# Performance work log

Measured on AMD Instinct MI355X. Metric: run time of the kernel, lower is better.

## Reference

```python
import jax, jax.numpy as jnp
import numpy as np

B, C, H, W = 2, 512, 128, 128
L_NUM, HEADS, LEVELS, POINTS = 6, 8, 1, 4
HEAD_DIM = C // HEADS


def setup_inputs() -> dict:
    key = jax.random.key(0)
    ks = jax.random.split(key, 16)
    s = 0.02
    rn = lambda k, shape, scale=s: jax.random.normal(k, shape, jnp.float32) * scale
    return dict(
        bev_feat=jax.random.normal(ks[0], (B, C, H, W), jnp.float32),
        lidar_feat=jax.random.normal(ks[1], (B, C, H, W), jnp.float32),
        Wv=rn(ks[2], (L_NUM, C, C)), bv=jnp.zeros((L_NUM, C), jnp.float32),
        Woff=rn(ks[3], (L_NUM, C, HEADS * LEVELS * POINTS * 2)),
        boff=rn(ks[4], (L_NUM, HEADS * LEVELS * POINTS * 2), 0.5),
        Waw=rn(ks[5], (L_NUM, C, HEADS * LEVELS * POINTS)),
        baw=jnp.zeros((L_NUM, HEADS * LEVELS * POINTS), jnp.float32),
        Wout=rn(ks[6], (L_NUM, C, C)), bout=jnp.zeros((L_NUM, C), jnp.float32),
        ln1_g=jnp.ones((L_NUM, C), jnp.float32), ln1_b=jnp.zeros((L_NUM, C), jnp.float32),
        W1=rn(ks[7], (L_NUM, C, C)), W2=rn(ks[8], (L_NUM, C, C)),
        ln2_g=jnp.ones((L_NUM, C), jnp.float32), ln2_b=jnp.zeros((L_NUM, C), jnp.float32),
        pe_W1=rn(ks[9], (2, C), 0.5),
        pe_bn_g=jnp.ones((C,), jnp.float32), pe_bn_b=jnp.zeros((C,), jnp.float32),
        pe_bn_m=jnp.zeros((C,), jnp.float32), pe_bn_v=jnp.ones((C,), jnp.float32),
        pe_W2=rn(ks[10], (C, C)),
    )


def _layer_norm(x, g, b):
    mu = jnp.mean(x, -1, keepdims=True)
    var = jnp.mean((x - mu) ** 2, -1, keepdims=True)
    return (x - mu) * jax.lax.rsqrt(var + 1e-5) * g + b


def _bilinear_gather(v_flat, locx, locy):
    # v_flat: (B, heads, H*W, d); locx/locy: (B, heads, S) normalized [0,1]
    # grid_sample semantics: align_corners=False, zero padding
    x = locx * W - 0.5
    y = locy * H - 0.5
    x0f = jnp.floor(x); y0f = jnp.floor(y)
    wx = x - x0f; wy = y - y0f
    x0 = x0f.astype(jnp.int32); y0 = y0f.astype(jnp.int32)

    def corner(xi, yi, w):
        inb = (xi >= 0) & (xi < W) & (yi >= 0) & (yi < H)
        idx = jnp.clip(yi, 0, H - 1) * W + jnp.clip(xi, 0, W - 1)
        g = jnp.take_along_axis(v_flat, idx[..., None], axis=2)
        return g * (w * inb)[..., None]

    return (corner(x0, y0, (1 - wx) * (1 - wy)) + corner(x0 + 1, y0, wx * (1 - wy))
            + corner(x0, y0 + 1, (1 - wx) * wy) + corner(x0 + 1, y0 + 1, wx * wy))


def reference(bev_feat, lidar_feat, Wv, bv, Woff, boff, Waw, baw, Wout, bout,
              ln1_g, ln1_b, W1, W2, ln2_g, ln2_b,
              pe_W1, pe_bn_g, pe_bn_b, pe_bn_m, pe_bn_v, pe_W2):
    N = H * W
    # sparse voxelization: keep rows with all-nonzero features, pack valid-first per batch
    lf = jnp.transpose(lidar_feat, (0, 2, 3, 1)).reshape(B, N, C)
    mask = jnp.all(lf != 0, axis=-1)                       # (B,N)
    order = jnp.argsort((~mask).astype(jnp.int32), axis=1, stable=True)  # valid first
    valid = jnp.take_along_axis(mask, order, axis=1)       # (B,N)
    q = jnp.take_along_axis(lf, order[..., None], axis=1) * valid[..., None]
    hh = jnp.arange(N) // W
    ww = jnp.arange(N) % W
    ref_all = jnp.stack([ww / W, hh / H], -1).astype(jnp.float32)  # (N,2) = (x,y)
    ref = jnp.broadcast_to(ref_all, (B, N, 2))
    ref = jnp.take_along_axis(ref, order[..., None], axis=1) * valid[..., None]
    # learned positional embedding (BatchNorm in eval mode)
    pe = ref.reshape(B * N, 2) @ pe_W1
    pe = (pe - pe_bn_m) * jax.lax.rsqrt(pe_bn_v + 1e-5) * pe_bn_g + pe_bn_b
    q_pos = (jax.nn.relu(pe) @ pe_W2).reshape(B, N, C)
    feat_flat = jnp.transpose(bev_feat.reshape(B, C, N), (0, 2, 1))  # (B,N,C)
    norm_xy = jnp.array([W, H], jnp.float32)  # offset normalizer per level (w,h)
    for i in range(L_NUM):
        ident = q
        x = q + q_pos
        v = (feat_flat @ Wv[i] + bv[i]).reshape(B, N, HEADS, HEAD_DIM)
        v_flat = jnp.transpose(v, (0, 2, 1, 3))  # (B,heads,N,d)
        off = (x @ Woff[i] + boff[i]).reshape(B, N, HEADS, LEVELS * POINTS, 2)
        aw = jax.nn.softmax((x @ Waw[i] + baw[i]).reshape(B, N, HEADS, LEVELS * POINTS), axis=-1)
        loc = ref[:, :, None, None, :] + off / norm_xy      # (B,N,heads,P,2)
        locx = jnp.transpose(loc[..., 0], (0, 2, 1, 3)).reshape(B, HEADS, N * POINTS)
        locy = jnp.transpose(loc[..., 1], (0, 2, 1, 3)).reshape(B, HEADS, N * POINTS)
        samp = _bilinear_gather(v_flat, locx, locy).reshape(B, HEADS, N, POINTS, HEAD_DIM)
        awt = jnp.transpose(aw, (0, 2, 1, 3))               # (B,heads,N,P)
        out = jnp.sum(samp * awt[..., None], axis=3)        # (B,heads,N,d)
        out = jnp.transpose(out, (0, 2, 1, 3)).reshape(B, N, C)
        q = out @ Wout[i] + bout[i] + ident                 # dropout in eval = identity
        q = _layer_norm(q, ln1_g[i], ln1_b[i])
        q = jax.nn.relu(q @ W1[i]) @ W2[i] + q
        q = _layer_norm(q, ln2_g[i], ln2_b[i])
    # scatter back to dense (B,C,H,W); invalid voxels stay zero
    slots = jnp.zeros((B, N, C), q.dtype)
    slots = slots.at[jnp.arange(B)[:, None], order].set(q * valid[..., None])
    return jnp.transpose(slots.reshape(B, H, W, C), (0, 3, 1, 2))
```

## Files before the change

### kernel.cpp

```cpp
#include <hip/hip_runtime.h>
#include <cstdint>
#include <cstddef>

#define BDIM 2
#define CDIM 512
#define HDIM 128
#define WDIM 128
#define NDIM (HDIM * WDIM)
#define LNUM 6
#define NHEADS 8
#define HEAD_DIM 64
#define NPTS 4
#define BN_TOT (BDIM * NDIM)

typedef unsigned short u16;
typedef __attribute__((ext_vector_type(8))) short bf16x8;
typedef __attribute__((ext_vector_type(4))) float f32x4;

__device__ __forceinline__ u16 f2bf(float x) {
    unsigned u = __float_as_uint(x);
    u += 0x7fffu + ((u >> 16) & 1u);
    return (u16)(u >> 16);
}
__device__ __forceinline__ float bf2f(u16 h) {
    return __uint_as_float(((unsigned)h) << 16);
}

__device__ __forceinline__ void load_lds16(const void* g, void* l) {
    __builtin_amdgcn_global_load_lds(
        (const __attribute__((address_space(1))) void*)g,
        (__attribute__((address_space(3))) void*)l, 16, 0, 0);
}

__global__ void mask_kernel(const float* __restrict__ lidar, int* __restrict__ mask)
{
    int idx = blockIdx.x * blockDim.x + threadIdx.x;
    if (idx >= BN_TOT) return;
    int b = idx / NDIM;
    int n = idx - b * NDIM;
    const float* p = lidar + (size_t)b * CDIM * NDIM + n;
    int ok = 1;
#pragma unroll 8
    for (int c = 0; c < CDIM; ++c)
        ok &= (p[(size_t)c * NDIM] != 0.0f);
    mask[idx] = ok;
}

__global__ void order_kernel(const int* __restrict__ mask, int* __restrict__ order,
                             int* __restrict__ nvalid)
{
    int b = blockIdx.x;
    const int* m = mask + b * NDIM;
    int* ord = order + b * NDIM;
    __shared__ int part[256];
    __shared__ int totalValid;
    int t = threadIdx.x;
    const int CHUNK = NDIM / 256;
    int base = t * CHUNK;
    int cnt = 0;
    for (int i = 0; i < CHUNK; ++i) cnt += m[base + i];
    part[t] = cnt;
    __syncthreads();
    for (int s = 1; s < 256; s <<= 1) {
        int v = (t >= s) ? part[t - s] : 0;
        __syncthreads();
        part[t] += v;
        __syncthreads();
    }
    if (t == 255) { totalValid = part[255]; nvalid[b] = part[255]; }
    __syncthreads();
    int validBefore = (t == 0) ? 0 : part[t - 1];
    int nv = totalValid;
    for (int i = 0; i < CHUNK; ++i) {
        int n = base + i;
        if (m[n]) { ord[validBefore] = n; validBefore++; }
        else      { int invBefore = n - validBefore; ord[nv + invBefore] = n; }
    }
}

__global__ void ref_kernel(const int* __restrict__ order, const int* __restrict__ nvalid,
                           float* __restrict__ ref)
{
    int idx = blockIdx.x * blockDim.x + threadIdx.x;
    if (idx >= BN_TOT) return;
    int b = idx / NDIM;
    int j = idx - b * NDIM;
    int n = order[idx];
    float flag = (j < nvalid[b]) ? 1.0f : 0.0f;
    int hh = n / WDIM;
    int ww = n - hh * WDIM;
    ref[(size_t)idx * 2 + 0] = ((float)ww / (float)WDIM) * flag;
    ref[(size_t)idx * 2 + 1] = ((float)hh / (float)HDIM) * flag;
}

__global__ void pack_q_kernel(const float* __restrict__ lidar, const int* __restrict__ order,
                              const int* __restrict__ nvalid, u16* __restrict__ q)
{
    __shared__ float tile[32][33];
    __shared__ int ord_s[32];
    int b  = blockIdx.z;
    int j0 = blockIdx.x * 32;
    int c0 = blockIdx.y * 32;
    int tx = threadIdx.x, ty = threadIdx.y;
    if (ty == 0) ord_s[tx] = order[b * NDIM + j0 + tx];
    __syncthreads();
    const float* src = lidar + (size_t)b * CDIM * NDIM;
#pragma unroll
    for (int k = 0; k < 4; ++k) {
        int cl = ty * 4 + k;
        tile[cl][tx] = src[(size_t)(c0 + cl) * NDIM + ord_s[tx]];
    }
    __syncthreads();
    int nv = nvalid[b];
#pragma unroll
    for (int k = 0; k < 4; ++k) {
        int jl = ty * 4 + k;
        int j = j0 + jl;
        float f = (j < nv) ? 1.0f : 0.0f;
        q[((size_t)b * NDIM + j) * CDIM + c0 + tx] = f2bf(tile[tx][jl] * f);
    }
}

__global__ void scatter_kernel(const u16* __restrict__ q, const int* __restrict__ order,
                               const int* __restrict__ nvalid, float* __restrict__ out)
{
    __shared__ float tile[32][33];
    __shared__ int ord_s[32];
    int b  = blockIdx.z;
    int j0 = blockIdx.x * 32;
    int c0 = blockIdx.y * 32;
    int tx = threadIdx.x, ty = threadIdx.y;
    if (ty == 0) ord_s[tx] = order[b * NDIM + j0 + tx];
    __syncthreads();
    int nv = nvalid[b];
#pragma unroll
    for (int k = 0; k < 4; ++k) {
        int jl = ty * 4 + k;
        int j = j0 + jl;
        float f = (j < nv) ? 1.0f : 0.0f;
        tile[jl][tx] = bf2f(q[((size_t)b * NDIM + j) * CDIM + c0 + tx]) * f;
    }
    __syncthreads();
    float* dst = out + (size_t)b * CDIM * NDIM;
#pragma unroll
    for (int k = 0; k < 4; ++k) {
        int cl = ty * 4 + k;
        dst[(size_t)(c0 + cl) * NDIM + ord_s[tx]] = tile[tx][cl];
    }
}

__global__ void tconv_b_kernel(const float* __restrict__ src0, u16* __restrict__ dst0)
{
    __shared__ float t[32][33];
    int z = blockIdx.z;
    const float* src = src0 + (size_t)z * 512 * 512;
    u16* dst = dst0 + (size_t)z * 512 * 512;
    int k0 = blockIdx.x * 32, n0 = blockIdx.y * 32;
    int tx = threadIdx.x, ty = threadIdx.y;
#pragma unroll
    for (int j = 0; j < 4; ++j) {
        int kl = ty * 4 + j;
        t[kl][tx] = src[(size_t)(k0 + kl) * 512 + n0 + tx];
    }
    __syncthreads();
#pragma unroll
    for (int j = 0; j < 4; ++j) {
        int nl = ty * 4 + j;
        dst[(size_t)(n0 + nl) * 512 + k0 + tx] = f2bf(t[tx][nl]);
    }
}

__global__ void tconv_offaw_b_kernel(const float* __restrict__ woff0,
                                     const float* __restrict__ waw0,
                                     u16* __restrict__ dst0)
{
    __shared__ float t[32][33];
    int z = blockIdx.z;
    const float* woff = woff0 + (size_t)z * 512 * 64;
    const float* waw  = waw0 + (size_t)z * 512 * 32;
    u16* dst = dst0 + (size_t)z * 96 * 512;
    int k0 = blockIdx.x * 32, n0 = blockIdx.y * 32;
    int tx = threadIdx.x, ty = threadIdx.y;
#pragma unroll
    for (int j = 0; j < 4; ++j) {
        int kl = ty * 4 + j;
        int n = n0 + tx;
        float v = (n < 64) ? woff[(size_t)(k0 + kl) * 64 + n]
                           : waw[(size_t)(k0 + kl) * 32 + (n - 64)];
        t[kl][tx] = v;
    }
    __syncthreads();
#pragma unroll
    for (int j = 0; j < 4; ++j) {
        int nl = ty * 4 + j;
        dst[(size_t)(n0 + nl) * 512 + k0 + tx] = f2bf(t[tx][nl]);
    }
}

__global__ void bev_conv_kernel(const float* __restrict__ bev, u16* __restrict__ dst)
{
    __shared__ float t[32][33];
    int b  = blockIdx.z;
    int n0 = blockIdx.x * 32;
    int c0 = blockIdx.y * 32;
    int tx = threadIdx.x, ty = threadIdx.y;
    const float* src = bev + (size_t)b * CDIM * NDIM;
#pragma unroll
    for (int j = 0; j < 4; ++j) {
        int cl = ty * 4 + j;
        t[cl][tx] = src[(size_t)(c0 + cl) * NDIM + n0 + tx];
    }
    __syncthreads();
#pragma unroll
    for (int j = 0; j < 4; ++j) {
        int nl = ty * 4 + j;
        dst[((size_t)b * NDIM + n0 + nl) * CDIM + c0 + tx] = f2bf(t[tx][nl]);
    }
}

__global__ void pe_hidden_kernel(const float* __restrict__ ref, const float* __restrict__ W1,
                                 const float* __restrict__ g, const float* __restrict__ bb,
                                 const float* __restrict__ m, const float* __restrict__ v,
                                 u16* __restrict__ out)
{
    int row = blockIdx.x;
    float r0 = ref[(size_t)row * 2 + 0];
    float r1 = ref[(size_t)row * 2 + 1];
    for (int c = threadIdx.x; c < CDIM; c += blockDim.x) {
        float pe = r0 * W1[c] + r1 * W1[CDIM + c];
        pe = (pe - m[c]) * rsqrtf(v[c] + 1e-5f) * g[c] + bb[c];
        out[(size_t)row * CDIM + c] = f2bf(fmaxf(pe, 0.0f));
    }
}

__global__ void add_bf_kernel(const u16* __restrict__ q, const u16* __restrict__ qpos,
                              u16* __restrict__ x)
{
    size_t i = (size_t)blockIdx.x * blockDim.x + threadIdx.x;
    uint4 qa = ((const uint4*)q)[i];
    uint4 pv = ((const uint4*)qpos)[i];
    unsigned qw[4] = {qa.x, qa.y, qa.z, qa.w};
    unsigned pw[4] = {pv.x, pv.y, pv.z, pv.w};
    unsigned rw[4];
#pragma unroll
    for (int k = 0; k < 4; ++k) {
        float a0 = bf2f((u16)(qw[k] & 0xffff)), a1 = bf2f((u16)(qw[k] >> 16));
        float p0 = bf2f((u16)(pw[k] & 0xffff)), p1 = bf2f((u16)(pw[k] >> 16));
        rw[k] = (unsigned)f2bf(a0 + p0) | ((unsigned)f2bf(a1 + p1) << 16);
    }
    uint4 r; r.x = rw[0]; r.y = rw[1]; r.z = rw[2]; r.w = rw[3];
    ((uint4*)x)[i] = r;
}

__global__ __launch_bounds__(256) void gemm_bf16(
    const u16* __restrict__ A, const u16* __restrict__ Bt,
    const float* __restrict__ bias, u16* __restrict__ outB, int relu)
{
    __shared__ u16 As[2][128 * 32];
    __shared__ u16 Bs[2][128 * 32];
    int tid = threadIdx.x;
    int wave = tid >> 6, lane = tid & 63;
    int wr = wave >> 1, wc = wave & 1;
    int quad = lane >> 4, l15 = lane & 15;
    int bm = blockIdx.y * 128, bn = blockIdx.x * 128;

    f32x4 acc[4][4];
#pragma unroll
    for (int i = 0; i < 4; ++i)
#pragma unroll
        for (int j = 0; j < 4; ++j) { f32x4 z = {0.f, 0.f, 0.f, 0.f}; acc[i][j] = z; }

    int e0 = wave * 512 + lane * 8;
    int e1 = (wave + 4) * 512 + lane * 8;
    const u16* Ag0 = A + (size_t)(bm + (e0 >> 5)) * 512 + (e0 & 31);
    const u16* Ag1 = A + (size_t)(bm + (e1 >> 5)) * 512 + (e1 & 31);
    const u16* Bg0 = Bt + (size_t)(bn + (e0 >> 5)) * 512 + (e0 & 31);
    const u16* Bg1 = Bt + (size_t)(bn + (e1 >> 5)) * 512 + (e1 & 31);

    load_lds16(Ag0, &As[0][wave * 512]);
    load_lds16(Ag1, &As[0][(wave + 4) * 512]);
    load_lds16(Bg0, &Bs[0][wave * 512]);
    load_lds16(Bg1, &Bs[0][(wave + 4) * 512]);

    for (int it = 0; it < 16; ++it) {
        __syncthreads();
        int cur = it & 1, nxt = cur ^ 1;
        if (it < 15) {
            int kn = (it + 1) * 32;
            load_lds16(Ag0 + kn, &As[nxt][wave * 512]);
            load_lds16(Ag1 + kn, &As[nxt][(wave + 4) * 512]);
            load_lds16(Bg0 + kn, &Bs[nxt][wave * 512]);
            load_lds16(Bg1 + kn, &Bs[nxt][(wave + 4) * 512]);
        }
        bf16x8 av[4], bv[4];
#pragma unroll
        for (int mi = 0; mi < 4; ++mi)
            av[mi] = *(const bf16x8*)&As[cur][(wr * 64 + mi * 16 + l15) * 32 + quad * 8];
#pragma unroll
        for (int ni = 0; ni < 4; ++ni)
            bv[ni] = *(const bf16x8*)&Bs[cur][(wc * 64 + ni * 16 + l15) * 32 + quad * 8];
#pragma unroll
        for (int mi = 0; mi < 4; ++mi)
#pragma unroll
            for (int ni = 0; ni < 4; ++ni)
                acc[mi][ni] = __builtin_amdgcn_mfma_f32_16x16x32_bf16(
                    av[mi], bv[ni], acc[mi][ni], 0, 0, 0);
    }

    int rowb = bm + wr * 64;
    int colb = bn + wc * 64;
#pragma unroll
    for (int mi = 0; mi < 4; ++mi) {
#pragma unroll
        for (int ni = 0; ni < 4; ++ni) {
            int col = colb + ni * 16 + l15;
            float bi = bias ? bias[col] : 0.0f;
#pragma unroll
            for (int r = 0; r < 4; ++r) {
                int row = rowb + mi * 16 + quad * 4 + r;
                float val = acc[mi][ni][r] + bi;
                if (relu) val = fmaxf(val, 0.0f);
                outB[(size_t)row * 512 + col] = f2bf(val);
            }
        }
    }
}

__global__ __launch_bounds__(512, 4) void gemm_ln(
    const u16* __restrict__ A, const u16* __restrict__ Bt,
    const float* __restrict__ bias, const u16* __restrict__ resid,
    const float* __restrict__ g, const float* __restrict__ bta,
    u16* __restrict__ outQ, const u16* __restrict__ qpos, u16* __restrict__ outX)
{
    __shared__ u16 As[2][64 * 32];
    __shared__ u16 Bs[2][512 * 32];
    __shared__ float rs[8][64];
    __shared__ float rq[8][64];
    __shared__ float muL[64], invL[64];

    int tid = threadIdx.x;
    int wv = tid >> 6, lane = tid & 63;
    int quad = lane >> 4, l15 = lane & 15;
    int bm = blockIdx.x * 64;

    f32x4 acc[4][4];
#pragma unroll
    for (int i = 0; i < 4; ++i)
#pragma unroll
        for (int j = 0; j < 4; ++j) { f32x4 z = {0.f, 0.f, 0.f, 0.f}; acc[i][j] = z; }

    const u16* Ag = A + (size_t)(bm + wv * 16 + (lane >> 2)) * 512 + (lane & 3) * 8;
    const u16* Bg[4];
#pragma unroll
    for (int it = 0; it < 4; ++it) {
        int s = wv * 4 + it;
        Bg[it] = Bt + (size_t)(s * 16 + (lane >> 2)) * 512 + (lane & 3) * 8;
    }

    if (wv < 4) load_lds16(Ag, &As[0][wv * 512]);
#pragma unroll
    for (int it = 0; it < 4; ++it) load_lds16(Bg[it], &Bs[0][(wv * 4 + it) * 512]);

    for (int kk = 0; kk < 16; ++kk) {
        __syncthreads();
        int cur = kk & 1, nxt = cur ^ 1;
        if (kk < 15) {
            int kn = (kk + 1) * 32;
            if (wv < 4) load_lds16(Ag + kn, &As[nxt][wv * 512]);
#pragma unroll
            for (int it = 0; it < 4; ++it)
                load_lds16(Bg[it] + kn, &Bs[nxt][(wv * 4 + it) * 512]);
        }
        bf16x8 av[4], bv[4];
#pragma unroll
        for (int mi = 0; mi < 4; ++mi)
            av[mi] = *(const bf16x8*)&As[cur][(mi * 16 + l15) * 32 + quad * 8];
#pragma unroll
        for (int ni = 0; ni < 4; ++ni)
            bv[ni] = *(const bf16x8*)&Bs[cur][(wv * 64 + ni * 16 + l15) * 32 + quad * 8];
#pragma unroll
        for (int mi = 0; mi < 4; ++mi)
#pragma unroll
            for (int ni = 0; ni < 4; ++ni)
                acc[mi][ni] = __builtin_amdgcn_mfma_f32_16x16x32_bf16(
                    av[mi], bv[ni], acc[mi][ni], 0, 0, 0);
    }

    int colb = wv * 64;
    float biasv[4], gv[4], btv[4];
#pragma unroll
    for (int ni = 0; ni < 4; ++ni) {
        int c = colb + ni * 16 + l15;
        biasv[ni] = bias ? bias[c] : 0.0f;
        gv[ni] = g[c];
        btv[ni] = bta[c];
    }
#pragma unroll
    for (int mi = 0; mi < 4; ++mi) {
#pragma unroll
        for (int r = 0; r < 4; ++r) {
            size_t rowoff = (size_t)(bm + mi * 16 + quad * 4 + r) * 512;
#pragma unroll
            for (int ni = 0; ni < 4; ++ni) {
                int col = colb + ni * 16 + l15;
                acc[mi][ni][r] += biasv[ni] + bf2f(resid[rowoff + col]);
            }
        }
    }
#pragma unroll
    for (int mi = 0; mi < 4; ++mi) {
#pragma unroll
        for (int r = 0; r < 4; ++r) {
            float s = acc[mi][0][r] + acc[mi][1][r] + acc[mi][2][r] + acc[mi][3][r];
            float s2 = acc[mi][0][r] * acc[mi][0][r] + acc[mi][1][r] * acc[mi][1][r]
                     + acc[mi][2][r] * acc[mi][2][r] + acc[mi][3][r] * acc[mi][3][r];
#pragma unroll
            for (int m = 1; m < 16; m <<= 1) {
                s  += __shfl_xor(s, m, 64);
                s2 += __shfl_xor(s2, m, 64);
            }
            if (l15 == 0) {
                rs[wv][mi * 16 + quad * 4 + r] = s;
                rq[wv][mi * 16 + quad * 4 + r] = s2;
            }
        }
    }
    __syncthreads();
    if (tid < 64) {
        float s = 0.f, s2 = 0.f;
#pragma unroll
        for (int w = 0; w < 8; ++w) { s += rs[w][tid]; s2 += rq[w][tid]; }
        float mu = s * (1.0f / 512.0f);
        float var = s2 * (1.0f / 512.0f) - mu * mu;
        muL[tid] = mu;
        invL[tid] = rsqrtf(var + 1e-5f);
    }
    __syncthreads();
#pragma unroll
    for (int mi = 0; mi < 4; ++mi) {
#pragma unroll
        for (int r = 0; r < 4; ++r) {
            int lrow = mi * 16 + quad * 4 + r;
            float mu = muL[lrow], iv = invL[lrow];
            size_t rowoff = (size_t)(bm + lrow) * 512;
#pragma unroll
            for (int ni = 0; ni < 4; ++ni) {
                int col = colb + ni * 16 + l15;
                float y = (acc[mi][ni][r] - mu) * iv * gv[ni] + btv[ni];
                outQ[rowoff + col] = f2bf(y);
                if (outX)
                    outX[rowoff + col] = f2bf(y + bf2f(qpos[rowoff + col]));
            }
        }
    }
}

__global__ __launch_bounds__(256) void gemm_offaw(
    const u16* __restrict__ A, const u16* __restrict__ Bt,
    const float* __restrict__ boff, const float* __restrict__ baw,
    u16* __restrict__ offb, u16* __restrict__ awb)
{
    __shared__ u16 As[2][128 * 32];
    __shared__ u16 Bs[2][128 * 32];
    int tid = threadIdx.x;
    int wave = tid >> 6, lane = tid & 63;
    int wr = wave >> 1, wc = wave & 1;
    int quad = lane >> 4, l15 = lane & 15;
    int bm = blockIdx.y * 128;

    f32x4 acc[4][4];
#pragma unroll
    for (int i = 0; i < 4; ++i)
#pragma unroll
        for (int j = 0; j < 4; ++j) { f32x4 z = {0.f, 0.f, 0.f, 0.f}; acc[i][j] = z; }

    int e0 = wave * 512 + lane * 8;
    int e1 = (wave + 4) * 512 + lane * 8;
    int br0 = e0 >> 5; if (br0 > 95) br0 = 95;
    int br1 = e1 >> 5; if (br1 > 95) br1 = 95;
    const u16* Ag0 = A + (size_t)(bm + (e0 >> 5)) * 512 + (e0 & 31);
    const u16* Ag1 = A + (size_t)(bm + (e1 >> 5)) * 512 + (e1 & 31);
    const u16* Bg0 = Bt + (size_t)br0 * 512 + (e0 & 31);
    const u16* Bg1 = Bt + (size_t)br1 * 512 + (e1 & 31);

    load_lds16(Ag0, &As[0][wave * 512]);
    load_lds16(Ag1, &As[0][(wave + 4) * 512]);
    load_lds16(Bg0, &Bs[0][wave * 512]);
    load_lds16(Bg1, &Bs[0][(wave + 4) * 512]);

    for (int it = 0; it < 16; ++it) {
        __syncthreads();
        int cur = it & 1, nxt = cur ^ 1;
        if (it < 15) {
            int kn = (it + 1) * 32;
            load_lds16(Ag0 + kn, &As[nxt][wave * 512]);
            load_lds16(Ag1 + kn, &As[nxt][(wave + 4) * 512]);
            load_lds16(Bg0 + kn, &Bs[nxt][wave * 512]);
            load_lds16(Bg1 + kn, &Bs[nxt][(wave + 4) * 512]);
        }
        bf16x8 av[4], bv[4];
#pragma unroll
        for (int mi = 0; mi < 4; ++mi)
            av[mi] = *(const bf16x8*)&As[cur][(wr * 64 + mi * 16 + l15) * 32 + quad * 8];
#pragma unroll
        for (int ni = 0; ni < 4; ++ni)
            bv[ni] = *(const bf16x8*)&Bs[cur][(wc * 64 + ni * 16 + l15) * 32 + quad * 8];
#pragma unroll
        for (int mi = 0; mi < 4; ++mi)
#pragma unroll
            for (int ni = 0; ni < 4; ++ni)
                acc[mi][ni] = __builtin_amdgcn_mfma_f32_16x16x32_bf16(
                    av[mi], bv[ni], acc[mi][ni], 0, 0, 0);
    }

    int rowb = bm + wr * 64;
#pragma unroll
    for (int mi = 0; mi < 4; ++mi) {
#pragma unroll
        for (int ni = 0; ni < 4; ++ni) {
            int col = wc * 64 + ni * 16 + l15;
            if (col < 96) {
                float bi = (col < 64) ? boff[col] : baw[col - 64];
#pragma unroll
                for (int r = 0; r < 4; ++r) {
                    int row = rowb + mi * 16 + quad * 4 + r;
                    float val = acc[mi][ni][r] + bi;
                    if (col < 64) offb[(size_t)row * 64 + col] = f2bf(val);
                    else          awb[(size_t)row * 32 + (col - 64)] = f2bf(val);
                }
            }
        }
    }
}

__global__ __launch_bounds__(256) void sample_kernel(
    const float* __restrict__ ref, const u16* __restrict__ off,
    const u16* __restrict__ aw, const u16* __restrict__ v,
    u16* __restrict__ out)
{
    int bj = blockIdx.x * 4 + (threadIdx.x >> 6);
    int lane = threadIdx.x & 63;
    int h  = lane >> 3;
    int d8 = (lane & 7) * 8;
    int b  = bj >> 14;

    float rx = ref[(size_t)bj * 2 + 0];
    float ry = ref[(size_t)bj * 2 + 1];
    uint4 offv = *(const uint4*)(off + (size_t)bj * 64 + h * 8);
    uint2 awv  = *(const uint2*)(aw + (size_t)bj * 32 + h * 4);

    float l0 = bf2f((u16)(awv.x & 0xffff)), l1 = bf2f((u16)(awv.x >> 16));
    float l2 = bf2f((u16)(awv.y & 0xffff)), l3 = bf2f((u16)(awv.y >> 16));
    float mx = fmaxf(fmaxf(l0, l1), fmaxf(l2, l3));
    float e[4];
    e[0] = expf(l0 - mx); e[1] = expf(l1 - mx);
    e[2] = expf(l2 - mx); e[3] = expf(l3 - mx);
    float inv_es = 1.0f / (e[0] + e[1] + e[2] + e[3]);

    const u16* vb = v + (size_t)b * NDIM * CDIM + h * HEAD_DIM + d8;
    float acc[8] = {0.f, 0.f, 0.f, 0.f, 0.f, 0.f, 0.f, 0.f};
    unsigned ow[4] = {offv.x, offv.y, offv.z, offv.w};

#pragma unroll
    for (int p = 0; p < NPTS; ++p) {
        float ox = bf2f((u16)(ow[p] & 0xffff));
        float oy = bf2f((u16)(ow[p] >> 16));
        float X = rx * (float)WDIM + ox - 0.5f;
        float Y = ry * (float)HDIM + oy - 0.5f;
        float x0f = floorf(X), y0f = floorf(Y);
        float wx = X - x0f, wy = Y - y0f;
        int x0 = (int)x0f, y0 = (int)y0f;
        float ep = e[p];
#pragma unroll
        for (int cy = 0; cy < 2; ++cy) {
            int yy = y0 + cy;
            float wyc = cy ? wy : (1.0f - wy);
            int yin = (yy >= 0) & (yy < HDIM);
            int yc = min(max(yy, 0), HDIM - 1);
#pragma unroll
            for (int cx = 0; cx < 2; ++cx) {
                int xx = x0 + cx;
                float wxc = cx ? wx : (1.0f - wx);
                int xin = (xx >= 0) & (xx < WDIM);
                int xc = min(max(xx, 0), WDIM - 1);
                float wgt = ep * wyc * wxc * (float)(yin & xin);
                uint4 vv = *(const uint4*)(vb + (size_t)(yc * WDIM + xc) * CDIM);
                acc[0] += wgt * bf2f((u16)(vv.x & 0xffff));
                acc[1] += wgt * bf2f((u16)(vv.x >> 16));
                acc[2] += wgt * bf2f((u16)(vv.y & 0xffff));
                acc[3] += wgt * bf2f((u16)(vv.y >> 16));
                acc[4] += wgt * bf2f((u16)(vv.z & 0xffff));
                acc[5] += wgt * bf2f((u16)(vv.z >> 16));
                acc[6] += wgt * bf2f((u16)(vv.w & 0xffff));
                acc[7] += wgt * bf2f((u16)(vv.w >> 16));
            }
        }
    }
    uint4 r;
    r.x = (unsigned)f2bf(acc[0] * inv_es) | ((unsigned)f2bf(acc[1] * inv_es) << 16);
    r.y = (unsigned)f2bf(acc[2] * inv_es) | ((unsigned)f2bf(acc[3] * inv_es) << 16);
    r.z = (unsigned)f2bf(acc[4] * inv_es) | ((unsigned)f2bf(acc[5] * inv_es) << 16);
    r.w = (unsigned)f2bf(acc[6] * inv_es) | ((unsigned)f2bf(acc[7] * inv_es) << 16);
    *(uint4*)(out + (size_t)bj * CDIM + h * HEAD_DIM + d8) = r;
}

extern "C" void kernel_launch(void* const* d_in, const int* in_sizes, int n_in,
                              void* d_out, int out_size, void* d_ws, size_t ws_size,
                              hipStream_t stream)
{
    const float* bev   = (const float*)d_in[0];
    const float* lidar = (const float*)d_in[1];
    const float* Wv    = (const float*)d_in[2];
    const float* bv    = (const float*)d_in[3];
    const float* Woff  = (const float*)d_in[4];
    const float* boff  = (const float*)d_in[5];
    const float* Waw   = (const float*)d_in[6];
    const float* baw   = (const float*)d_in[7];
    const float* Wout  = (const float*)d_in[8];
    const float* bout  = (const float*)d_in[9];
    const float* ln1g  = (const float*)d_in[10];
    const float* ln1b  = (const float*)d_in[11];
    const float* W1    = (const float*)d_in[12];
    const float* W2    = (const float*)d_in[13];
    const float* ln2g  = (const float*)d_in[14];
    const float* ln2b  = (const float*)d_in[15];
    const float* peW1  = (const float*)d_in[16];
    const float* peg   = (const float*)d_in[17];
    const float* peb   = (const float*)d_in[18];
    const float* pem   = (const float*)d_in[19];
    const float* pev   = (const float*)d_in[20];
    const float* peW2  = (const float*)d_in[21];

    const size_t NC = (size_t)BN_TOT * CDIM;
    const size_t WSZ = 512 * 512;

    char* base = (char*)d_ws;
    u16* q      = (u16*)base;
    u16* actA   = (u16*)(base + NC * 2);
    u16* actB   = (u16*)(base + NC * 4);
    u16* wt     = (u16*)(base + NC * 6);
    u16* wtv    = wt;
    u16* wtout  = wt + 6 * WSZ;
    u16* wt1    = wt + 12 * WSZ;
    u16* wt2    = wt + 18 * WSZ;
    u16* wtpe   = wt + 24 * WSZ;
    u16* offawt = wt + 25 * WSZ;
    u16* offb   = offawt + 6 * 96 * 512;
    u16* awb    = offb + (size_t)BN_TOT * 64;
    float* refb = (float*)(awb + (size_t)BN_TOT * 32);
    int* mask   = (int*)(refb + (size_t)BN_TOT * 2);
    int* order  = mask + BN_TOT;
    int* nvalid = order + BN_TOT;

    u16* qpos_bf = (u16*)d_out;
    u16* featT   = (u16*)d_out + NC;

    dim3 blk328(32, 8);
    dim3 gemm_grid(4, 256);
    dim3 offaw_grid(1, 256);
    int  ln_grid = BN_TOT / 64;

    mask_kernel<<<BN_TOT / 256, 256, 0, stream>>>(lidar, mask);
    order_kernel<<<BDIM, 256, 0, stream>>>(mask, order, nvalid);
    ref_kernel<<<BN_TOT / 256, 256, 0, stream>>>(order, nvalid, refb);
    pack_q_kernel<<<dim3(NDIM / 32, CDIM / 32, BDIM), blk328, 0, stream>>>(lidar, order, nvalid, q);
    bev_conv_kernel<<<dim3(NDIM / 32, CDIM / 32, BDIM), blk328, 0, stream>>>(bev, featT);

    tconv_b_kernel<<<dim3(16, 16, 6), blk328, 0, stream>>>(Wv,   wtv);
    tconv_b_kernel<<<dim3(16, 16, 6), blk328, 0, stream>>>(Wout, wtout);
    tconv_b_kernel<<<dim3(16, 16, 6), blk328, 0, stream>>>(W1,   wt1);
    tconv_b_kernel<<<dim3(16, 16, 6), blk328, 0, stream>>>(W2,   wt2);
    tconv_b_kernel<<<dim3(16, 16, 1), blk328, 0, stream>>>(peW2, wtpe);
    tconv_offaw_b_kernel<<<dim3(16, 3, 6), blk328, 0, stream>>>(Woff, Waw, offawt);

    pe_hidden_kernel<<<BN_TOT, 128, 0, stream>>>(refb, peW1, peg, peb, pem, pev, actA);
    gemm_bf16<<<gemm_grid, 256, 0, stream>>>(actA, wtpe, nullptr, qpos_bf, 0);

    add_bf_kernel<<<(unsigned)(NC / 8 / 256), 256, 0, stream>>>(q, qpos_bf, actB);

    for (int i = 0; i < LNUM; ++i) {
        gemm_offaw<<<offaw_grid, 256, 0, stream>>>(actB, offawt + (size_t)i * 96 * 512,
                                                   boff + i * 64, baw + i * 32, offb, awb);
        gemm_bf16<<<gemm_grid, 256, 0, stream>>>(featT, wtv + (size_t)i * WSZ,
                                                 bv + i * CDIM, actA, 0);
        sample_kernel<<<BN_TOT / 4, 256, 0, stream>>>(refb, offb, awb, actA, actB);
        gemm_ln<<<ln_grid, 512, 0, stream>>>(actB, wtout + (size_t)i * WSZ, bout + i * CDIM,
                                             q, ln1g + i * CDIM, ln1b + i * CDIM,
                                             q, nullptr, nullptr);
        gemm_bf16<<<gemm_grid, 256, 0, stream>>>(q, wt1 + (size_t)i * WSZ, nullptr, actA, 1);
        gemm_ln<<<ln_grid, 512, 0, stream>>>(actA, wt2 + (size_t)i * WSZ, nullptr,
                                             q, ln2g + i * CDIM, ln2b + i * CDIM,
                                             q, qpos_bf,
                                             (i < LNUM - 1) ? actB : nullptr);
    }

    scatter_kernel<<<dim3(NDIM / 32, CDIM / 32, BDIM), blk328, 0, stream>>>(
        q, order, nvalid, (float*)d_out);
}
```

Before: 1.878 ms.

## Make each wave load its own GEMM tile rows and drop block-wide vmcnt waits

In three bf16 GEMM kernels, each wave now copies from global memory into LDS exactly the A/B rows it later reads, so it only has to wait on its own outstanding loads. The full __syncthreads is replaced by a bare s_barrier plus an explicit s_waitcnt vmcnt(8), which keeps the next stage's prefetch in flight while the current stage is computed. This is meant to cut stall time at each k-step barrier. The cost is redundant loads: A rows are fetched twice in the 2x2 kernels and by all waves in the LN kernel, and correctness now depends on the hand-written vmcnt counts and the wave-private data layout.

```diff
diff --git a/kernel.cpp b/kernel.cpp
--- a/kernel.cpp
+++ b/kernel.cpp
@@ -31,6 +31,9 @@
         (const __attribute__((address_space(1))) void*)g,
         (__attribute__((address_space(3))) void*)l, 16, 0, 0);
 }
+
+__device__ __forceinline__ void wait_vm8() { asm volatile("s_waitcnt vmcnt(8)" ::: "memory"); }
+__device__ __forceinline__ void wait_vm0() { asm volatile("s_waitcnt vmcnt(0)" ::: "memory"); }
 
 __global__ void mask_kernel(const float* __restrict__ lidar, int* __restrict__ mask)
 {
@@ -270,27 +273,33 @@
 #pragma unroll
         for (int j = 0; j < 4; ++j) { f32x4 z = {0.f, 0.f, 0.f, 0.f}; acc[i][j] = z; }
 
-    int e0 = wave * 512 + lane * 8;
-    int e1 = (wave + 4) * 512 + lane * 8;
-    const u16* Ag0 = A + (size_t)(bm + (e0 >> 5)) * 512 + (e0 & 31);
-    const u16* Ag1 = A + (size_t)(bm + (e1 >> 5)) * 512 + (e1 & 31);
-    const u16* Bg0 = Bt + (size_t)(bn + (e0 >> 5)) * 512 + (e0 & 31);
-    const u16* Bg1 = Bt + (size_t)(bn + (e1 >> 5)) * 512 + (e1 & 31);
-
-    load_lds16(Ag0, &As[0][wave * 512]);
-    load_lds16(Ag1, &As[0][(wave + 4) * 512]);
-    load_lds16(Bg0, &Bs[0][wave * 512]);
-    load_lds16(Bg1, &Bs[0][(wave + 4) * 512]);
+    const u16* Ag[4];
+    const u16* Bg[4];
+#pragma unroll
+    for (int s = 0; s < 4; ++s) {
+        Ag[s] = A  + (size_t)(bm + wr * 64 + s * 16 + (lane >> 2)) * 512 + (lane & 3) * 8;
+        Bg[s] = Bt + (size_t)(bn + wc * 64 + s * 16 + (lane >> 2)) * 512 + (lane & 3) * 8;
+    }
+
+#pragma unroll
+    for (int s = 0; s < 4; ++s) {
+        load_lds16(Ag[s], &As[0][(wr * 4 + s) * 512]);
+        load_lds16(Bg[s], &Bs[0][(wc * 4 + s) * 512]);
+    }
 
     for (int it = 0; it < 16; ++it) {
-        __syncthreads();
+        __builtin_amdgcn_s_barrier();
         int cur = it & 1, nxt = cur ^ 1;
         if (it < 15) {
             int kn = (it + 1) * 32;
-            load_lds16(Ag0 + kn, &As[nxt][wave * 512]);
-            load_lds16(Ag1 + kn, &As[nxt][(wave + 4) * 512]);
-            load_lds16(Bg0 + kn, &Bs[nxt][wave * 512]);
-            load_lds16(Bg1 + kn, &Bs[nxt][(wave + 4) * 512]);
+#pragma unroll
+            for (int s = 0; s < 4; ++s) {
+                load_lds16(Ag[s] + kn, &As[nxt][(wr * 4 + s) * 512]);
+                load_lds16(Bg[s] + kn, &Bs[nxt][(wc * 4 + s) * 512]);
+            }
+            wait_vm8();
+        } else {
+            wait_vm0();
         }
         bf16x8 av[4], bv[4];
 #pragma unroll
@@ -349,27 +358,33 @@
 #pragma unroll
         for (int j = 0; j < 4; ++j) { f32x4 z = {0.f, 0.f, 0.f, 0.f}; acc[i][j] = z; }
 
-    const u16* Ag = A + (size_t)(bm + wv * 16 + (lane >> 2)) * 512 + (lane & 3) * 8;
+    const u16* Ag[4];
     const u16* Bg[4];
 #pragma unroll
-    for (int it = 0; it < 4; ++it) {
-        int s = wv * 4 + it;
-        Bg[it] = Bt + (size_t)(s * 16 + (lane >> 2)) * 512 + (lane & 3) * 8;
-    }
-
-    if (wv < 4) load_lds16(Ag, &As[0][wv * 512]);
-#pragma unroll
-    for (int it = 0; it < 4; ++it) load_lds16(Bg[it], &Bs[0][(wv * 4 + it) * 512]);
+    for (int s = 0; s < 4; ++s) {
+        Ag[s] = A  + (size_t)(bm + s * 16 + (lane >> 2)) * 512 + (lane & 3) * 8;
+        Bg[s] = Bt + (size_t)((wv * 4 + s) * 16 + (lane >> 2)) * 512 + (lane & 3) * 8;
+    }
+
+#pragma unroll
+    for (int s = 0; s < 4; ++s) {
+        load_lds16(Ag[s], &As[0][s * 512]);
+        load_lds16(Bg[s], &Bs[0][(wv * 4 + s) * 512]);
+    }
 
     for (int kk = 0; kk < 16; ++kk) {
-        __syncthreads();
+        __builtin_amdgcn_s_barrier();
         int cur = kk & 1, nxt = cur ^ 1;
         if (kk < 15) {
             int kn = (kk + 1) * 32;
-            if (wv < 4) load_lds16(Ag + kn, &As[nxt][wv * 512]);
-#pragma unroll
-            for (int it = 0; it < 4; ++it)
-                load_lds16(Bg[it] + kn, &Bs[nxt][(wv * 4 + it) * 512]);
+#pragma unroll
+            for (int s = 0; s < 4; ++s) {
+                load_lds16(Ag[s] + kn, &As[nxt][s * 512]);
+                load_lds16(Bg[s] + kn, &Bs[nxt][(wv * 4 + s) * 512]);
+            }
+            wait_vm8();
+        } else {
+            wait_vm0();
         }
         bf16x8 av[4], bv[4];
 #pragma unroll
@@ -474,29 +489,35 @@
 #pragma unroll
         for (int j = 0; j < 4; ++j) { f32x4 z = {0.f, 0.f, 0.f, 0.f}; acc[i][j] = z; }
 
-    int e0 = wave * 512 + lane * 8;
-    int e1 = (wave + 4) * 512 + lane * 8;
-    int br0 = e0 >> 5; if (br0 > 95) br0 = 95;
-    int br1 = e1 >> 5; if (br1 > 95) br1 = 95;
-    const u16* Ag0 = A + (size_t)(bm + (e0 >> 5)) * 512 + (e0 & 31);
-    const u16* Ag1 = A + (size_t)(bm + (e1 >> 5)) * 512 + (e1 & 31);
-    const u16* Bg0 = Bt + (size_t)br0 * 512 + (e0 & 31);
-    const u16* Bg1 = Bt + (size_t)br1 * 512 + (e1 & 31);
-
-    load_lds16(Ag0, &As[0][wave * 512]);
-    load_lds16(Ag1, &As[0][(wave + 4) * 512]);
-    load_lds16(Bg0, &Bs[0][wave * 512]);
-    load_lds16(Bg1, &Bs[0][(wave + 4) * 512]);
+    const u16* Ag[4];
+    const u16* Bg[4];
+#pragma unroll
+    for (int s = 0; s < 4; ++s) {
+        Ag[s] = A + (size_t)(bm + wr * 64 + s * 16 + (lane >> 2)) * 512 + (lane & 3) * 8;
+        int br = wc * 64 + s * 16 + (lane >> 2);
+        if (br > 95) br = 95;
+        Bg[s] = Bt + (size_t)br * 512 + (lane & 3) * 8;
+    }
+
+#pragma unroll
+    for (int s = 0; s < 4; ++s) {
+        load_lds16(Ag[s], &As[0][(wr * 4 + s) * 512]);
+        load_lds16(Bg[s], &Bs[0][(wc * 4 + s) * 512]);
+    }
 
     for (int it = 0; it < 16; ++it) {
-        __syncthreads();
+        __builtin_amdgcn_s_barrier();
         int cur = it & 1, nxt = cur ^ 1;
         if (it < 15) {
             int kn = (it + 1) * 32;
-            load_lds16(Ag0 + kn, &As[nxt][wave * 512]);
-            load_lds16(Ag1 + kn, &As[nxt][(wave + 4) * 512]);
-            load_lds16(Bg0 + kn, &Bs[nxt][wave * 512]);
-            load_lds16(Bg1 + kn, &Bs[nxt][(wave + 4) * 512]);
+#pragma unroll
+            for (int s = 0; s < 4; ++s) {
+                load_lds16(Ag[s] + kn, &As[nxt][(wr * 4 + s) * 512]);
+                load_lds16(Bg[s] + kn, &Bs[nxt][(wc * 4 + s) * 512]);
+            }
+            wait_vm8();
+        } else {
+            wait_vm0();
         }
         bf16x8 av[4], bv[4];
 #pragma unroll
```

Result: no change. 1.864 ms (-0.7%).
